# Optimization experiments

Measured on AMD Instinct MI355X. Metric: run time of the kernel, lower is better.

The kernel has to match this reference:

```python
import jax, jax.numpy as jnp
import numpy as np

N_HEAD = 16
ROPE_BASE = 10000.0


def _rope(x):
    # x: (B, T, H, D), interleaved even/odd (GPT-NeoX style)
    B, T, H, D = x.shape
    inv_freq = 1.0 / (ROPE_BASE ** (jnp.arange(0, D, 2, dtype=jnp.float32) / D))
    t = jnp.arange(T, dtype=jnp.float32)
    freqs = t[:, None] * inv_freq[None, :]            # (T, D//2)
    cos = jnp.cos(freqs)[None, :, None, :]            # (1, T, 1, D//2)
    sin = jnp.sin(freqs)[None, :, None, :]
    x1, x2 = x[..., ::2], x[..., 1::2]
    y1 = x1 * cos - x2 * sin
    y2 = x1 * sin + x2 * cos
    return jnp.stack((y1, y2), axis=-1).reshape(B, T, H, D)


def setup_inputs() -> dict:
    key = jax.random.key(0)
    k1, k2, k3 = jax.random.split(key, 3)
    B, T, C = 4, 2048, 1024
    x = jax.random.normal(k1, (B, T, C), dtype=jnp.float32)
    W_attn = jax.random.normal(k2, (C, 3 * C), dtype=jnp.float32) * (1.0 / np.sqrt(C))
    W_proj = jax.random.normal(k3, (C, C), dtype=jnp.float32) * (1.0 / np.sqrt(C))
    return {"x": x, "W_attn": W_attn, "W_proj": W_proj}


def reference(x, W_attn, W_proj):
    B, T, C = x.shape
    H = N_HEAD
    D = C // H
    qkv = jnp.einsum('btc,cf->btf', x, W_attn)        # (B, T, 3C)
    q, k, v = jnp.split(qkv, 3, axis=-1)
    q = _rope(q.reshape(B, T, H, D))
    k = _rope(k.reshape(B, T, H, D))
    v = v.reshape(B, T, H, D)
    # (B, H, T, D)
    q = q.transpose(0, 2, 1, 3)
    k = k.transpose(0, 2, 1, 3)
    v = v.transpose(0, 2, 1, 3)
    scale = 1.0 / np.sqrt(D).astype(np.float32)
    scores = jnp.einsum('bhqd,bhkd->bhqk', q, k) * scale
    causal = jnp.tril(jnp.ones((T, T), dtype=bool))
    scores = jnp.where(causal[None, None], scores, jnp.finfo(scores.dtype).min)
    att = jax.nn.softmax(scores, axis=-1)
    y = jnp.einsum('bhqk,bhkd->bhqd', att, v)         # (B, H, T, D)
    y = y.transpose(0, 2, 1, 3).reshape(B, T, C)
    return jnp.einsum('btc,cf->btf', y, W_proj)
```

## Files before the change

### kernel.cpp

```cpp
#include <hip/hip_runtime.h>
#include <hip/hip_bf16.h>
#include <math.h>

typedef __attribute__((ext_vector_type(8))) __bf16 bf16x8;
typedef __attribute__((ext_vector_type(4))) float f32x4;
typedef __attribute__((ext_vector_type(16))) float f32x16;
typedef __attribute__((ext_vector_type(4))) unsigned short us4;

#define DEVINL static __device__ __forceinline__

DEVINL unsigned short f2bf(float f) {
  union { float f; unsigned int u; } v; v.f = f;
  return (unsigned short)((v.u + 0x7FFFu + ((v.u >> 16) & 1u)) >> 16);
}

DEVINL unsigned short f2bf_hw(float f) {
  __bf16 h = (__bf16)f;
  union { __bf16 h; unsigned short u; } v; v.h = h;
  return v.u;
}

DEVINL unsigned pk2(float a, float b) {
  return (unsigned)f2bf_hw(a) | ((unsigned)f2bf_hw(b) << 16);
}

DEVINL f32x4 mfma16(bf16x8 a, bf16x8 b, f32x4 c) {
  return __builtin_amdgcn_mfma_f32_16x16x32_bf16(a, b, c, 0, 0, 0);
}
DEVINL f32x16 mfma32(bf16x8 a, bf16x8 b, f32x16 c) {
  return __builtin_amdgcn_mfma_f32_32x32x16_bf16(a, b, c, 0, 0, 0);
}

#define GLOAD16(GP, LP)                                                        \
  __builtin_amdgcn_global_load_lds(                                            \
      (const __attribute__((address_space(1))) void*)(GP),                     \
      (__attribute__((address_space(3))) void*)(LP), 16, 0, 0)

static constexpr int kB = 4, kT = 2048, kC = 1024, kH = 16, kD = 64;
static constexpr int kM = kB * kT;

__global__ __launch_bounds__(256) void prep_kernel(
    const float* __restrict__ x, unsigned short* __restrict__ xb,
    const float* __restrict__ Wa, unsigned short* __restrict__ WaT,
    const float* __restrict__ Wp, unsigned short* __restrict__ WpT,
    float* __restrict__ cosT, float* __restrict__ sinT) {
  const int blk = blockIdx.x;
  if (blk < 2048) {
    const int n4 = kM * kC / 4;
    for (int i = blk * 256 + threadIdx.x; i < n4; i += 2048 * 256) {
      float4 v = ((const float4*)x)[i];
      us4 o;
      o[0] = f2bf(v.x); o[1] = f2bf(v.y); o[2] = f2bf(v.z); o[3] = f2bf(v.w);
      ((us4*)xb)[i] = o;
    }
  } else if (blk < 2048 + 3072 + 1024) {
    __shared__ float tile[32][33];
    int t = blk - 2048;
    const float* W; unsigned short* WT; int N, bx, by;
    if (t < 3072) { W = Wa; WT = WaT; N = 3072; bx = t % 96; by = t / 96; }
    else { t -= 3072; W = Wp; WT = WpT; N = 1024; bx = t % 32; by = t / 32; }
    const int n0 = bx * 32, k0 = by * 32;
    const int tx = threadIdx.x & 31, ty = threadIdx.x >> 5;
#pragma unroll
    for (int i = 0; i < 4; ++i)
      tile[ty + i * 8][tx] = W[(size_t)(k0 + ty + i * 8) * N + n0 + tx];
    __syncthreads();
#pragma unroll
    for (int i = 0; i < 4; ++i)
      WT[(size_t)(n0 + ty + i * 8) * 1024 + k0 + tx] = f2bf(tile[tx][ty + i * 8]);
  } else {
    int idx = (blk - 6144) * 256 + threadIdx.x;
    int d2 = idx >> 11, t = idx & 2047;
    double ang = (double)t * pow(10000.0, -(double)d2 / 32.0);
    cosT[idx] = (float)cos(ang);
    sinT[idx] = (float)sin(ang);
  }
}

template <int EPI>
__global__ __launch_bounds__(512, 2) void gemm_bt_kernel(
    const unsigned short* __restrict__ A, const unsigned short* __restrict__ Bt,
    float* __restrict__ Cout, int Ndim, int Kdim,
    const float* __restrict__ cosT, const float* __restrict__ sinT,
    unsigned short* __restrict__ Qr, unsigned short* __restrict__ Kr,
    unsigned short* __restrict__ Vtg) {
  __shared__ unsigned short As[3][256 * 64];
  __shared__ unsigned short Bs[3][128 * 64];
  const int tid = threadIdx.x;
  const int wave = tid >> 6, lane = tid & 63;

  const int nwg = gridDim.x * gridDim.y;
  const int lin = blockIdx.y * gridDim.x + blockIdx.x;
  const int wg = (lin & 7) * (nwg >> 3) + (lin >> 3);
  const int n0 = (wg % gridDim.x) * 128, m0 = (wg / gridDim.x) * 256;

  const int wr = wave >> 1, wc = wave & 1;

  f32x4 acc[4][4] = {};

  const int fr = lane & 15;

  const int sblk = tid;
  const int srow3 = sblk >> 3, skb = sblk & 7;
  const int sgran = (skb ^ (srow3 & 7)) << 3;

  auto stageA = [&](int t, int l) {
    const int bb = t % 3;
    const int k0 = t << 6;
    const int row = (l << 6) + srow3;
    GLOAD16(A + (size_t)(m0 + row) * Kdim + k0 + sgran,
            &As[bb][(l * 512 + wave * 64) * 8]);
  };
  auto stageB = [&](int t, int l) {
    const int bb = t % 3;
    const int k0 = t << 6;
    const int row = (l << 6) + srow3;
    GLOAD16(Bt + (size_t)(n0 + row) * Kdim + k0 + sgran,
            &Bs[bb][(l * 512 + wave * 64) * 8]);
  };

  const int NT = Kdim >> 6;

  stageA(0, 0); stageA(0, 1); stageA(0, 2); stageA(0, 3);
  stageB(0, 0); stageB(0, 1);
  stageA(1, 0); stageA(1, 1); stageA(1, 2); stageA(1, 3);
  stageB(1, 0); stageB(1, 1);
  asm volatile("s_waitcnt vmcnt(6)" ::: "memory");
  __builtin_amdgcn_sched_barrier(0);
  __builtin_amdgcn_s_barrier();

  const int rx = lane & 7, ku = lane >> 4;

  for (int t = 0; t < NT; ++t) {
    const int buf = t % 3;
    const unsigned char* Ab = (const unsigned char*)As[buf];
    const unsigned char* Bb = (const unsigned char*)Bs[buf];
    bf16x8 af[4], bfr[4];

    {
      const int col = ((ku ^ rx) << 4);
#pragma unroll
      for (int f = 0; f < 4; ++f)
        af[f] = *(const bf16x8*)(Ab + (wr * 64 + f * 16 + fr) * 128 + col);
#pragma unroll
      for (int f = 0; f < 4; ++f)
        bfr[f] = *(const bf16x8*)(Bb + (wc * 64 + f * 16 + fr) * 128 + col);
    }
    if (t + 2 < NT) { stageA(t + 2, 0); stageA(t + 2, 1); stageB(t + 2, 0); }
    __builtin_amdgcn_s_barrier();
    asm volatile("s_waitcnt lgkmcnt(0)" ::: "memory");
    __builtin_amdgcn_sched_barrier(0);
    __builtin_amdgcn_s_setprio(1);
#pragma unroll
    for (int i = 0; i < 4; ++i)
#pragma unroll
      for (int j = 0; j < 4; ++j)
        acc[i][j] = mfma16(af[i], bfr[j], acc[i][j]);
    __builtin_amdgcn_s_setprio(0);
    __builtin_amdgcn_s_barrier();

    {
      const int col = (((4 | ku) ^ rx) << 4);
#pragma unroll
      for (int f = 0; f < 4; ++f)
        af[f] = *(const bf16x8*)(Ab + (wr * 64 + f * 16 + fr) * 128 + col);
#pragma unroll
      for (int f = 0; f < 4; ++f)
        bfr[f] = *(const bf16x8*)(Bb + (wc * 64 + f * 16 + fr) * 128 + col);
    }
    if (t + 2 < NT) { stageA(t + 2, 2); stageA(t + 2, 3); stageB(t + 2, 1); }
    if (t + 2 < NT) {
      asm volatile("s_waitcnt vmcnt(6)" ::: "memory");
    } else if (t + 1 < NT) {
      asm volatile("s_waitcnt vmcnt(0)" ::: "memory");
    }
    __builtin_amdgcn_sched_barrier(0);
    __builtin_amdgcn_s_barrier();
    asm volatile("s_waitcnt lgkmcnt(0)" ::: "memory");
    __builtin_amdgcn_sched_barrier(0);
    __builtin_amdgcn_s_setprio(1);
#pragma unroll
    for (int i = 0; i < 4; ++i)
#pragma unroll
      for (int j = 0; j < 4; ++j)
        acc[i][j] = mfma16(af[i], bfr[j], acc[i][j]);
    __builtin_amdgcn_s_setprio(0);
    __builtin_amdgcn_s_barrier();
  }

  const int lr = (lane >> 4) * 4;
  const int fc = lane & 15;
  if (EPI == 0) {
#pragma unroll
    for (int i = 0; i < 4; ++i) {
      int mb = m0 + wr * 64 + i * 16 + lr;
#pragma unroll
      for (int j = 0; j < 4; ++j) {
        int n = n0 + wc * 64 + j * 16 + fc;
#pragma unroll
        for (int r = 0; r < 4; ++r)
          Cout[(size_t)(mb + r) * Ndim + n] = acc[i][j][r];
      }
    }
  } else {
#pragma unroll
    for (int i = 0; i < 4; ++i) {
      int mb = m0 + wr * 64 + i * 16 + lr;
      int b = mb >> 11, t0 = mb & 2047;
#pragma unroll
      for (int j = 0; j < 4; ++j) {
        int n = n0 + wc * 64 + j * 16 + fc;
        int sec = n >> 10;
        int c = n & 1023;
        int h = c >> 6, d = c & 63;
        size_t bh = (size_t)(b * 16 + h);
        if (sec == 2) {
          us4 pk;
#pragma unroll
          for (int r = 0; r < 4; ++r) pk[r] = f2bf(acc[i][j][r]);
          *(us4*)&Vtg[(bh * 64 + d) * 2048 + t0] = pk;
        } else {
          unsigned short* dst = (sec == 0) ? Qr : Kr;
          float4 c4 = *(const float4*)&cosT[(d >> 1) * 2048 + t0];
          float4 s4 = *(const float4*)&sinT[(d >> 1) * 2048 + t0];
          const float* cp = (const float*)&c4;
          const float* sp = (const float*)&s4;
#pragma unroll
          for (int r = 0; r < 4; ++r) {
            float v = acc[i][j][r];
            float pv = __shfl_xor(v, 1);
            float y = (d & 1) ? fmaf(pv, sp[r], v * cp[r])
                              : fmaf(v, cp[r], -pv * sp[r]);
            dst[(bh * 2048 + t0 + r) * 64 + d] = f2bf(y);
          }
        }
      }
    }
  }
}

__global__ __launch_bounds__(128, 2)
void attn_kernel(const unsigned short* __restrict__ Qr,
                 const unsigned short* __restrict__ Kr,
                 const unsigned short* __restrict__ Vtg,
                 unsigned short* __restrict__ Yb) {
  __shared__ unsigned short Ks[2][64 * 64];
  __shared__ unsigned short Vs[2][64 * 64];

  const int tid = threadIdx.x;
  const int wave = tid >> 6, lane = tid & 63;
  const int q31 = lane & 31, hi = lane >> 5;
  const int srow = lane >> 3;
  const int sblk = (lane & 7) ^ srow;
  const int rswz = (lane & 7) << 4;

  int lin = blockIdx.y * 8 + blockIdx.x;
  int wg = (lin & 7) * 128 + (lin >> 3);
  const int cpair = wg & 15;
  const int bh = wg >> 4;

  const unsigned short* Qg = Qr + (size_t)bh * 2048 * 64;
  const unsigned short* Kg = Kr + (size_t)bh * 2048 * 64;
  const unsigned short* Vg = Vtg + (size_t)bh * 64 * 2048;

  const float c = 0.18033688f;
  const float THR = 44.0f;

  auto stage = [&](int j, int bb) {
    int kv0s = j * 64;
#pragma unroll
    for (int o = 0; o < 4; ++o) {
      int s = o * 2 + wave;
      int row = s * 8 + srow;
      GLOAD16(Kg + ((size_t)(kv0s + row) * 64 + sblk * 8), &Ks[bb][s * 512]);
      GLOAD16(Vg + ((size_t)row * 2048 + kv0s + sblk * 8), &Vs[bb][s * 512]);
    }
  };

  for (int seg = 0; seg < 2; ++seg) {
    const int qb = seg ? (31 - cpair) : cpair;
    const int qw = qb * 64 + wave * 32;
    const int qg = qw + q31;
    const int NT = qb + 1;

    bf16x8 qf[4];
#pragma unroll
    for (int ds = 0; ds < 4; ++ds)
      qf[ds] = *(const bf16x8*)&Qg[(size_t)qg * 64 + ds * 16 + hi * 8];

    float mrow = -1e30f, lrow = 0.f;
    f32x16 y0 = {}, y1 = {};

    stage(0, 0);
    asm volatile("s_waitcnt vmcnt(0)" ::: "memory");
    __syncthreads();

    for (int t = 0; t < NT; ++t) {
      const int buf = t & 1;
      if (t + 1 < NT) stage(t + 1, buf ^ 1);
      const int kv0 = t * 64;

      if (kv0 <= qw + 31) {
        f32x16 st[2] = {};
        __builtin_amdgcn_s_setprio(1);
#pragma unroll
        for (int sub = 0; sub < 2; ++sub) {
          const unsigned char* kbase =
              (const unsigned char*)Ks[buf] + (sub * 32 + q31) * 128;
#pragma unroll
          for (int ds = 0; ds < 4; ++ds) {
            bf16x8 af = *(const bf16x8*)(kbase + ((ds * 32 + hi * 16) ^ rswz));
            st[sub] = mfma32(af, qf[ds], st[sub]);
          }
        }
        __builtin_amdgcn_s_setprio(0);

        if (kv0 + 63 > qw) {
#pragma unroll
          for (int sub = 0; sub < 2; ++sub)
#pragma unroll
            for (int r = 0; r < 16; ++r) {
              int kv = kv0 + sub * 32 + (r & 3) + 8 * (r >> 2) + 4 * hi;
              if (kv > qg) st[sub][r] = -1e30f;
            }
        }

        float tm = st[0][0];
#pragma unroll
        for (int r = 1; r < 16; ++r) tm = fmaxf(tm, st[0][r]);
#pragma unroll
        for (int r = 0; r < 16; ++r) tm = fmaxf(tm, st[1][r]);
        tm = fmaxf(tm, __shfl_xor(tm, 32));

        if (!__all(tm <= mrow + THR)) {
          float mn = fmaxf(mrow, tm);
          float al = __builtin_amdgcn_exp2f((mrow - mn) * c);
          mrow = mn;
          lrow *= al;
#pragma unroll
          for (int r = 0; r < 16; ++r) { y0[r] *= al; y1[r] *= al; }
        }

        const float mc = mrow * c;
        float ps = 0.f;
        unsigned pkw[2][8];
#pragma unroll
        for (int sub = 0; sub < 2; ++sub)
#pragma unroll
          for (int j = 0; j < 8; ++j) {
            float pa = __builtin_amdgcn_exp2f(fmaf(st[sub][2 * j], c, -mc));
            float pb = __builtin_amdgcn_exp2f(fmaf(st[sub][2 * j + 1], c, -mc));
            ps += pa + pb;
            pkw[sub][j] = pk2(pa, pb);
          }
        ps += __shfl_xor(ps, 32);
        lrow += ps;

        __builtin_amdgcn_s_setprio(1);
#pragma unroll
        for (int sub = 0; sub < 2; ++sub) {
#pragma unroll
          for (int ksl = 0; ksl < 2; ++ksl) {
            unsigned w0 = pkw[sub][ksl * 4 + 0], w2 = pkw[sub][ksl * 4 + 2];
            unsigned w1 = pkw[sub][ksl * 4 + 1], w3 = pkw[sub][ksl * 4 + 3];
            asm volatile("v_permlane32_swap_b32 %0, %1" : "+v"(w0), "+v"(w2));
            asm volatile("v_permlane32_swap_b32 %0, %1" : "+v"(w1), "+v"(w3));
            union { bf16x8 v; unsigned u[4]; } pf;
            pf.u[0] = w0; pf.u[1] = w1; pf.u[2] = w2; pf.u[3] = w3;
            const int cb = sub * 64 + ksl * 32 + hi * 16;
#pragma unroll
            for (int dm = 0; dm < 2; ++dm) {
              const int row = dm * 32 + q31;
              bf16x8 vf = *(const bf16x8*)((const unsigned char*)Vs[buf] +
                                           row * 128 + (cb ^ rswz));
              if (dm == 0) y0 = mfma32(vf, pf.v, y0);
              else         y1 = mfma32(vf, pf.v, y1);
            }
          }
        }
        __builtin_amdgcn_s_setprio(0);
      }

      __syncthreads();
    }

    const int b = bh >> 4, h = bh & 15;
    float inv = __builtin_amdgcn_rcpf(lrow);
    unsigned short* yrow = Yb + (size_t)(b * 2048 + qg) * 1024 + h * 64;
#pragma unroll
    for (int dm = 0; dm < 2; ++dm)
#pragma unroll
      for (int g = 0; g < 4; ++g) {
        us4 o;
#pragma unroll
        for (int e = 0; e < 4; ++e) {
          float yv = dm ? y1[g * 4 + e] : y0[g * 4 + e];
          o[e] = f2bf_hw(yv * inv);
        }
        *(us4*)&yrow[dm * 32 + g * 8 + hi * 4] = o;
      }
  }
}

extern "C" void kernel_launch(void* const* d_in, const int* in_sizes, int n_in,
                              void* d_out, int out_size, void* d_ws,
                              size_t ws_size, hipStream_t stream) {
  const float* x = (const float*)d_in[0];
  const float* Wa = (const float*)d_in[1];
  const float* Wp = (const float*)d_in[2];
  float* out = (float*)d_out;
  char* ws = (char*)d_ws;

  constexpr size_t OFF_WAT = 0;
  constexpr size_t OFF_WPT = 6291456;
  constexpr size_t OFF_COS = 8388608;
  constexpr size_t OFF_SIN = 8650752;
  constexpr size_t OFF_XB  = 8912896;
  constexpr size_t OFF_Q   = 25690112;
  constexpr size_t OFF_K   = 42467328;
  constexpr size_t OFF_V   = 59244544;

  unsigned short* WaT = (unsigned short*)(ws + OFF_WAT);
  unsigned short* WpT = (unsigned short*)(ws + OFF_WPT);
  float* cosT = (float*)(ws + OFF_COS);
  float* sinT = (float*)(ws + OFF_SIN);
  unsigned short* xb = (unsigned short*)(ws + OFF_XB);
  unsigned short* Yb = xb;
  unsigned short* Qr = (unsigned short*)(ws + OFF_Q);
  unsigned short* Kr = (unsigned short*)(ws + OFF_K);
  unsigned short* Vt = (unsigned short*)(ws + OFF_V);

  prep_kernel<<<2048 + 3072 + 1024 + 256, 256, 0, stream>>>(
      x, xb, Wa, WaT, Wp, WpT, cosT, sinT);

  gemm_bt_kernel<1><<<dim3(24, 32), 512, 0, stream>>>(
      xb, WaT, nullptr, 3072, 1024, cosT, sinT, Qr, Kr, Vt);

  attn_kernel<<<dim3(8, 128), 128, 0, stream>>>(Qr, Kr, Vt, Yb);

  gemm_bt_kernel<0><<<dim3(8, 32), 512, 0, stream>>>(
      Yb, WpT, out, 1024, 1024, nullptr, nullptr, nullptr, nullptr, nullptr);
}
```

Baseline: 181.1 us.

## Add 256x256-tile QKV GEMM with 8-phase ping-pong LDS pipeline

Replaces the generic 256x128 QKV projection GEMM with a dedicated kernel using 256x256 tiles, 8 waves arranged 2x4, and a double-buffered LDS schedule. The schedule interleaves global-to-LDS staging of half-tiles with four MFMA sub-phases per K-step, each separated by barriers. The larger tile raises arithmetic intensity per LDS byte and halves the grid to 384 blocks. In exchange it uses more registers (8x4 accumulators) and 128KB of LDS, and 384 blocks may underfill or unevenly load the CUs. The generic GEMM loses its fused RoPE epilogue and is now used only for the output projection.

Result: slower. 186.1 us (+2.8%).

```diff
diff --git a/kernel.cpp b/kernel.cpp
--- a/kernel.cpp
+++ b/kernel.cpp
@@ -77,13 +77,171 @@
   }
 }
 
+__global__ __launch_bounds__(512, 2) void qkv_gemm8_kernel(
+    const unsigned short* __restrict__ A, const unsigned short* __restrict__ Bt,
+    const float* __restrict__ cosT, const float* __restrict__ sinT,
+    unsigned short* __restrict__ Qr, unsigned short* __restrict__ Kr,
+    unsigned short* __restrict__ Vtg) {
+  __shared__ unsigned short As[2][256 * 64];
+  __shared__ unsigned short Bs[2][256 * 64];
+  const int tid = threadIdx.x;
+  const int wave = tid >> 6, lane = tid & 63;
+  const int Kdim = 1024;
+
+  const int lin = blockIdx.y * gridDim.x + blockIdx.x;
+  const int wg = (lin & 7) * 48 + (lin >> 3);
+  const int n0 = (wg % 12) * 256, m0 = (wg / 12) * 256;
+
+  const int wr = wave >> 2, wc = wave & 3;
+  const int fr = lane & 15, ku = lane >> 4, rx = lane & 7;
+  const int srow8 = lane >> 3;
+  const int sgk = (rx ^ srow8) << 3;
+
+  f32x4 acc[8][4] = {};
+  bf16x8 a[4][2], b0[2][2], b1[2][2];
+
+  auto stageA = [&](int t, int mh, int l) {
+    const int rb = l * 128 + mh * 64 + wave * 8;
+    GLOAD16(A + (size_t)(m0 + rb + srow8) * Kdim + (t << 6) + sgk,
+            &As[t & 1][rb * 64]);
+  };
+  auto stageB = [&](int t, int nh, int l) {
+    const int rb = l * 128 + (wave >> 2) * 64 + nh * 32 + (wave & 3) * 8;
+    GLOAD16(Bt + (size_t)(n0 + rb + srow8) * Kdim + (t << 6) + sgk,
+            &Bs[t & 1][rb * 64]);
+  };
+  auto readA = [&](int bb, int mh) {
+#pragma unroll
+    for (int i = 0; i < 4; ++i)
+#pragma unroll
+      for (int kh = 0; kh < 2; ++kh) {
+        const int row = wr * 128 + mh * 64 + i * 16 + fr;
+        a[i][kh] = *(const bf16x8*)((const unsigned char*)As[bb] + row * 128 +
+                                    ((((kh << 2) | ku) ^ rx) << 4));
+      }
+  };
+  auto readB = [&](int bb, int nh, bf16x8 (&bx)[2][2]) {
+#pragma unroll
+    for (int j = 0; j < 2; ++j)
+#pragma unroll
+      for (int kh = 0; kh < 2; ++kh) {
+        const int row = wc * 64 + nh * 32 + j * 16 + fr;
+        bx[j][kh] = *(const bf16x8*)((const unsigned char*)Bs[bb] + row * 128 +
+                                     ((((kh << 2) | ku) ^ rx) << 4));
+      }
+  };
+  auto mm = [&](int mh, bf16x8 (&bx)[2][2], int nh) {
+#pragma unroll
+    for (int kh = 0; kh < 2; ++kh)
+#pragma unroll
+      for (int i = 0; i < 4; ++i)
+#pragma unroll
+        for (int j = 0; j < 2; ++j)
+          acc[mh * 4 + i][nh * 2 + j] =
+              mfma16(a[i][kh], bx[j][kh], acc[mh * 4 + i][nh * 2 + j]);
+  };
+
+#define MIDBAR()                                          \
+  __builtin_amdgcn_sched_barrier(0);                      \
+  __builtin_amdgcn_s_barrier();                           \
+  asm volatile("s_waitcnt lgkmcnt(0)" ::: "memory");      \
+  __builtin_amdgcn_sched_barrier(0);                      \
+  __builtin_amdgcn_s_setprio(1)
+#define ENDBAR()                                          \
+  __builtin_amdgcn_s_setprio(0);                          \
+  __builtin_amdgcn_s_barrier()
+
+  const int NT = 16, NI = 8;
+
+  stageA(0, 0, 0); stageA(0, 0, 1);
+  stageB(0, 1, 0); stageB(0, 1, 1);
+  stageB(0, 0, 0); stageB(0, 0, 1);
+  stageA(0, 1, 0); stageA(0, 1, 1);
+  stageA(1, 0, 0); stageA(1, 0, 1);
+  stageB(1, 1, 0); stageB(1, 1, 1);
+  asm volatile("s_waitcnt vmcnt(4)" ::: "memory");
+  __builtin_amdgcn_sched_barrier(0);
+  __builtin_amdgcn_s_barrier();
+
+  for (int I = 0; I < NI; ++I) {
+    const int v = 2 * I + 1, w = 2 * I + 2, x = 2 * I + 3;
+
+    readA(0, 0); readB(0, 0, b0);
+    stageB(v, 0, 0); stageB(v, 0, 1);
+    MIDBAR(); mm(0, b0, 0); ENDBAR();
+    readB(0, 1, b1);
+    stageA(v, 1, 0); stageA(v, 1, 1);
+    MIDBAR(); mm(0, b1, 1); ENDBAR();
+    readA(0, 1);
+    if (w < NT) { stageA(w, 0, 0); stageA(w, 0, 1); }
+    MIDBAR(); mm(1, b1, 1); ENDBAR();
+    if (w < NT) {
+      stageB(w, 1, 0); stageB(w, 1, 1);
+      asm volatile("s_waitcnt vmcnt(4)" ::: "memory");
+    } else {
+      asm volatile("s_waitcnt vmcnt(0)" ::: "memory");
+    }
+    MIDBAR(); mm(1, b0, 0); ENDBAR();
+
+    readA(1, 0); readB(1, 0, b0);
+    if (w < NT) { stageB(w, 0, 0); stageB(w, 0, 1); }
+    MIDBAR(); mm(0, b0, 0); ENDBAR();
+    readB(1, 1, b1);
+    if (w < NT) { stageA(w, 1, 0); stageA(w, 1, 1); }
+    MIDBAR(); mm(0, b1, 1); ENDBAR();
+    readA(1, 1);
+    if (x < NT) { stageA(x, 0, 0); stageA(x, 0, 1); }
+    MIDBAR(); mm(1, b1, 1); ENDBAR();
+    if (x < NT) {
+      stageB(x, 1, 0); stageB(x, 1, 1);
+      asm volatile("s_waitcnt vmcnt(4)" ::: "memory");
+    }
+    MIDBAR(); mm(1, b0, 0); ENDBAR();
+  }
+#undef MIDBAR
+#undef ENDBAR
+
+  const int lr = (lane >> 4) * 4;
+  const int fc = lane & 15;
+#pragma unroll
+  for (int i = 0; i < 8; ++i) {
+    int mb = m0 + wr * 128 + i * 16 + lr;
+    int b = mb >> 11, t0 = mb & 2047;
+#pragma unroll
+    for (int j = 0; j < 4; ++j) {
+      int n = n0 + wc * 64 + j * 16 + fc;
+      int sec = n >> 10;
+      int c = n & 1023;
+      int h = c >> 6, d = c & 63;
+      size_t bh = (size_t)(b * 16 + h);
+      if (sec == 2) {
+        us4 pk;
+#pragma unroll
+        for (int r = 0; r < 4; ++r) pk[r] = f2bf(acc[i][j][r]);
+        *(us4*)&Vtg[(bh * 64 + d) * 2048 + t0] = pk;
+      } else {
+        unsigned short* dst = (sec == 0) ? Qr : Kr;
+        float4 c4 = *(const float4*)&cosT[(d >> 1) * 2048 + t0];
+        float4 s4 = *(const float4*)&sinT[(d >> 1) * 2048 + t0];
+        const float* cp = (const float*)&c4;
+        const float* sp = (const float*)&s4;
+#pragma unroll
+        for (int r = 0; r < 4; ++r) {
+          float vv = acc[i][j][r];
+          float pv = __shfl_xor(vv, 1);
+          float y = (d & 1) ? fmaf(pv, sp[r], vv * cp[r])
+                            : fmaf(vv, cp[r], -pv * sp[r]);
+          dst[(bh * 2048 + t0 + r) * 64 + d] = f2bf(y);
+        }
+      }
+    }
+  }
+}
+
 template <int EPI>
 __global__ __launch_bounds__(512, 2) void gemm_bt_kernel(
     const unsigned short* __restrict__ A, const unsigned short* __restrict__ Bt,
-    float* __restrict__ Cout, int Ndim, int Kdim,
-    const float* __restrict__ cosT, const float* __restrict__ sinT,
-    unsigned short* __restrict__ Qr, unsigned short* __restrict__ Kr,
-    unsigned short* __restrict__ Vtg) {
+    float* __restrict__ Cout, int Ndim, int Kdim) {
   __shared__ unsigned short As[3][256 * 64];
   __shared__ unsigned short Bs[3][128 * 64];
   const int tid = threadIdx.x;
@@ -99,7 +257,6 @@
   f32x4 acc[4][4] = {};
 
   const int fr = lane & 15;
-
   const int sblk = tid;
   const int srow3 = sblk >> 3, skb = sblk & 7;
   const int sgran = (skb ^ (srow3 & 7)) << 3;
@@ -190,51 +347,15 @@
 
   const int lr = (lane >> 4) * 4;
   const int fc = lane & 15;
-  if (EPI == 0) {
-#pragma unroll
-    for (int i = 0; i < 4; ++i) {
-      int mb = m0 + wr * 64 + i * 16 + lr;
-#pragma unroll
-      for (int j = 0; j < 4; ++j) {
-        int n = n0 + wc * 64 + j * 16 + fc;
-#pragma unroll
-        for (int r = 0; r < 4; ++r)
-          Cout[(size_t)(mb + r) * Ndim + n] = acc[i][j][r];
-      }
-    }
-  } else {
-#pragma unroll
-    for (int i = 0; i < 4; ++i) {
-      int mb = m0 + wr * 64 + i * 16 + lr;
-      int b = mb >> 11, t0 = mb & 2047;
-#pragma unroll
-      for (int j = 0; j < 4; ++j) {
-        int n = n0 + wc * 64 + j * 16 + fc;
-        int sec = n >> 10;
-        int c = n & 1023;
-        int h = c >> 6, d = c & 63;
-        size_t bh = (size_t)(b * 16 + h);
-        if (sec == 2) {
-          us4 pk;
-#pragma unroll
-          for (int r = 0; r < 4; ++r) pk[r] = f2bf(acc[i][j][r]);
-          *(us4*)&Vtg[(bh * 64 + d) * 2048 + t0] = pk;
-        } else {
-          unsigned short* dst = (sec == 0) ? Qr : Kr;
-          float4 c4 = *(const float4*)&cosT[(d >> 1) * 2048 + t0];
-          float4 s4 = *(const float4*)&sinT[(d >> 1) * 2048 + t0];
-          const float* cp = (const float*)&c4;
-          const float* sp = (const float*)&s4;
-#pragma unroll
-          for (int r = 0; r < 4; ++r) {
-            float v = acc[i][j][r];
-            float pv = __shfl_xor(v, 1);
-            float y = (d & 1) ? fmaf(pv, sp[r], v * cp[r])
-                              : fmaf(v, cp[r], -pv * sp[r]);
-            dst[(bh * 2048 + t0 + r) * 64 + d] = f2bf(y);
-          }
-        }
-      }
+#pragma unroll
+  for (int i = 0; i < 4; ++i) {
+    int mb = m0 + wr * 64 + i * 16 + lr;
+#pragma unroll
+    for (int j = 0; j < 4; ++j) {
+      int n = n0 + wc * 64 + j * 16 + fc;
+#pragma unroll
+      for (int r = 0; r < 4; ++r)
+        Cout[(size_t)(mb + r) * Ndim + n] = acc[i][j][r];
     }
   }
 }
@@ -433,11 +554,11 @@
   prep_kernel<<<2048 + 3072 + 1024 + 256, 256, 0, stream>>>(
       x, xb, Wa, WaT, Wp, WpT, cosT, sinT);
 
-  gemm_bt_kernel<1><<<dim3(24, 32), 512, 0, stream>>>(
-      xb, WaT, nullptr, 3072, 1024, cosT, sinT, Qr, Kr, Vt);
+  qkv_gemm8_kernel<<<dim3(12, 32), 512, 0, stream>>>(
+      xb, WaT, cosT, sinT, Qr, Kr, Vt);
 
   attn_kernel<<<dim3(8, 128), 128, 0, stream>>>(Qr, Kr, Vt, Yb);
 
   gemm_bt_kernel<0><<<dim3(8, 32), 512, 0, stream>>>(
-      Yb, WpT, out, 1024, 1024, nullptr, nullptr, nullptr, nullptr, nullptr);
-}
+      Yb, WpT, out, 1024, 1024);
+}
```
